# Performance work log

Measured on AMD Instinct MI355X. Metric: run time of the kernel, lower is better.

Reference implementation:

```python
import jax, jax.numpy as jnp
import numpy as np

N_VOCAB = 100000
N_FIELDS = 40
K = 64
ATTN = 64
BATCH = 2048

def setup_inputs() -> dict:
    key = jax.random.key(0)
    ks = jax.random.split(key, 9)
    x = jax.random.randint(ks[0], (BATCH, N_FIELDS), 0, N_VOCAB)
    lin_table = jax.random.normal(ks[1], (N_VOCAB, 1), dtype=jnp.float32) * 0.01
    V_table = jax.random.normal(ks[2], (N_VOCAB, K), dtype=jnp.float32) * 0.01
    W1 = jax.random.normal(ks[3], (K, ATTN), dtype=jnp.float32) * (1.0 / np.sqrt(K))
    b1 = jnp.zeros((ATTN,), dtype=jnp.float32)
    W2 = jax.random.normal(ks[4], (ATTN, 1), dtype=jnp.float32) * (1.0 / np.sqrt(ATTN))
    b2 = jnp.zeros((1,), dtype=jnp.float32)
    Wf = jax.random.normal(ks[5], (K, 1), dtype=jnp.float32) * (1.0 / np.sqrt(K))
    bf = jnp.zeros((1,), dtype=jnp.float32)
    return {"x": x, "lin_table": lin_table, "V_table": V_table,
            "W1": W1, "b1": b1, "W2": W2, "b2": b2, "Wf": Wf, "bf": bf}

def reference(x, lin_table, V_table, W1, b1, W2, b2, Wf, bf):
    # linear part: sum of per-feature scalar weights -> [B, 1]
    linear_part = jnp.sum(lin_table[x], axis=1)
    # embeddings: [B, F, K]
    embd = V_table[x]
    # pairwise interactions: [B, F, F, K]
    pw = embd[:, :, None, :] * embd[:, None, :, :]
    # attention MLP: k -> attn -> 1, scores [B, F, F, 1]
    h = jax.nn.relu(jnp.einsum('bijk,ka->bija', pw, W1) + b1)
    scores = jnp.einsum('bija,ao->bijo', h, W2) + b2
    # softmax over dim=2 (second field axis)
    probs = jax.nn.softmax(scores, axis=2)
    # weighted sum over j then i -> [B, K]
    weighted = jnp.sum(probs * pw, axis=2)
    weighted_embd = jnp.sum(weighted, axis=1)
    interaction_part = weighted_embd @ Wf + bf  # [B, 1]
    return jax.nn.sigmoid(linear_part + interaction_part)[:, 0]
```

## Files before the change

### kernel.cpp

```cpp
#include <hip/hip_runtime.h>

#define NF 40
#define KD 64

typedef float f32x4 __attribute__((ext_vector_type(4)));
typedef _Float16 f16x8 __attribute__((ext_vector_type(8)));
typedef _Float16 f16x4 __attribute__((ext_vector_type(4)));

__global__ __launch_bounds__(256, 4)
void afm_kernel(const int* __restrict__ x,
                const float* __restrict__ lin_table,
                const float* __restrict__ V_table,
                const float* __restrict__ W1,
                const float* __restrict__ b1,
                const float* __restrict__ W2,
                const float* __restrict__ b2,
                const float* __restrict__ Wf,
                const float* __restrict__ bf,
                float* __restrict__ out)
{
    __shared__ _Float16 ew[4][NF][72];
    __shared__ _Float16 Qw[4][48][72];
    __shared__ unsigned short lut[832];

    const int tid = threadIdx.x;
    const int w = tid >> 6;
    const int lane = tid & 63;
    const int l15 = lane & 15;
    const int lhi = lane >> 4;
    const int smp = blockIdx.x * 4 + w;

    for (int p0 = tid; p0 < 832; p0 += 256) {
        int p = p0 > 819 ? 819 : p0;
        int i = (int)((81.0f - sqrtf(6561.0f - 8.0f * (float)p)) * 0.5f);
        int off = (i * (81 - i)) >> 1;
        if ((((i + 1) * (80 - i)) >> 1) <= p) { ++i; off = (i * (81 - i)) >> 1; }
        else if (off > p)                     { --i; off = (i * (81 - i)) >> 1; }
        lut[p0] = (unsigned short)((i << 8) | (i + (p - off)));
    }

    _Float16* e = &ew[w][0][0];
    _Float16* Q = &Qw[w][0][0];

    {
        f16x8 zh = {0, 0, 0, 0, 0, 0, 0, 0};
        for (int t = lane; t < 192; t += 64) {
            if (t < 120) {
                int r = t / 3, c8 = t - r * 3;
                *reinterpret_cast<f16x8*>(Q + r * 72 + 40 + c8 * 8) = zh;
            } else {
                int t2 = t - 120, r9 = t2 / 9;
                *reinterpret_cast<f16x8*>(Q + (40 + r9) * 72 + (t2 - r9 * 9) * 8) = zh;
            }
        }
    }

    for (int q = lane; q < NF * (KD / 4); q += 64) {
        int i = q >> 4, k4 = q & 15;
        int ix = x[smp * NF + i];
        float4 v = reinterpret_cast<const float4*>(V_table + (size_t)ix * KD)[k4];
        f16x4 hv = {(_Float16)v.x, (_Float16)v.y, (_Float16)v.z, (_Float16)v.w};
        *reinterpret_cast<f16x4*>(e + i * 72 + k4 * 4) = hv;
    }
    float linv = (lane < NF) ? lin_table[x[smp * NF + lane]] : 0.0f;

    f16x8 Af[4][2];
    #pragma unroll
    for (int at = 0; at < 4; ++at) {
        #pragma unroll
        for (int ks = 0; ks < 2; ++ks) {
            f16x8 t;
            #pragma unroll
            for (int el = 0; el < 8; ++el)
                t[el] = (_Float16)W1[(ks * 32 + lhi * 8 + el) * KD + at * 16 + l15];
            Af[at][ks] = t;
        }
    }
    f32x4 b1v[4], w2v[4];
    #pragma unroll
    for (int at = 0; at < 4; ++at) {
        b1v[at] = *reinterpret_cast<const f32x4*>(b1 + at * 16 + lhi * 4);
        w2v[at] = *reinterpret_cast<const f32x4*>(W2 + at * 16 + lhi * 4);
    }
    float wfv[4];
    #pragma unroll
    for (int nt = 0; nt < 4; ++nt) wfv[nt] = Wf[nt * 16 + l15];
    const float bf0 = bf[0];

    __syncthreads();
    __builtin_amdgcn_wave_barrier();

    const int k0 = lhi * 8;
    for (int mt = 0; mt < 52; ++mt) {
        const int v = lut[mt * 16 + l15];
        const int i = v >> 8;
        const int j = v & 255;
        const _Float16* ei = e + i * 72;
        const _Float16* ej = e + j * 72;
        f16x8 B0 = (*reinterpret_cast<const f16x8*>(ei + k0)) *
                   (*reinterpret_cast<const f16x8*>(ej + k0));
        f16x8 B1 = (*reinterpret_cast<const f16x8*>(ei + k0 + 32)) *
                   (*reinterpret_cast<const f16x8*>(ej + k0 + 32));

        f32x4 d[4];
        #pragma unroll
        for (int at = 0; at < 4; ++at) {
            d[at] = b1v[at];
            d[at] = __builtin_amdgcn_mfma_f32_16x16x32_f16(Af[at][0], B0, d[at], 0, 0, 0);
            d[at] = __builtin_amdgcn_mfma_f32_16x16x32_f16(Af[at][1], B1, d[at], 0, 0, 0);
        }

        float s = 0.0f;
        #pragma unroll
        for (int at = 0; at < 4; ++at) {
            #pragma unroll
            for (int r = 0; r < 4; ++r)
                s = fmaf(fmaxf(d[at][r], 0.0f), w2v[at][r], s);
        }
        s += __shfl_xor(s, 16, 64);
        s += __shfl_xor(s, 32, 64);
        float qv = __expf(s);
        if (lhi == 0) {
            _Float16 qh = (_Float16)qv;
            Q[i * 72 + j] = qh;
            Q[j * 72 + i] = qh;
        }
    }
    __builtin_amdgcn_wave_barrier();

    float acc4[4] = {0.f, 0.f, 0.f, 0.f};
    #pragma unroll
    for (int mt = 0; mt < 3; ++mt) {
        const _Float16* qrow = Q + (mt * 16 + l15) * 72;
        f16x8 aq0 = *reinterpret_cast<const f16x8*>(qrow + lhi * 8);
        f16x8 aq1 = *reinterpret_cast<const f16x8*>(qrow + 32 + lhi * 8);

        f16x8 one0, one1;
        #pragma unroll
        for (int el = 0; el < 8; ++el) {
            one0[el] = (_Float16)1.0f;
            one1[el] = (lhi == 0) ? (_Float16)1.0f : (_Float16)0.0f;
        }
        f32x4 dz = {0.f, 0.f, 0.f, 0.f};
        dz = __builtin_amdgcn_mfma_f32_16x16x32_f16(aq0, one0, dz, 0, 0, 0);
        dz = __builtin_amdgcn_mfma_f32_16x16x32_f16(aq1, one1, dz, 0, 0, 0);
        float rz[4];
        #pragma unroll
        for (int r = 0; r < 4; ++r) {
            int ii = mt * 16 + lhi * 4 + r;
            rz[r] = (ii < NF) ? __builtin_amdgcn_rcpf(dz[r]) : 0.0f;
        }

        #pragma unroll
        for (int nt = 0; nt < 4; ++nt) {
            const int c = nt * 16 + l15;
            f16x8 bv0, bv1;
            #pragma unroll
            for (int el = 0; el < 8; ++el) {
                bv0[el] = e[(lhi * 8 + el) * 72 + c];
                bv1[el] = (lhi == 0) ? e[(32 + el) * 72 + c]
                                     : (_Float16)0.0f;
            }
            f32x4 dq = {0.f, 0.f, 0.f, 0.f};
            dq = __builtin_amdgcn_mfma_f32_16x16x32_f16(aq0, bv0, dq, 0, 0, 0);
            dq = __builtin_amdgcn_mfma_f32_16x16x32_f16(aq1, bv1, dq, 0, 0, 0);

            float a = 0.0f;
            #pragma unroll
            for (int r = 0; r < 4; ++r) {
                int ii = mt * 16 + lhi * 4 + r;
                int iic = ii > 39 ? 39 : ii;
                a = fmaf((float)e[iic * 72 + c] * dq[r], rz[r], a);
            }
            acc4[nt] += a;
        }
    }

    #pragma unroll
    for (int nt = 0; nt < 4; ++nt) {
        acc4[nt] += __shfl_xor(acc4[nt], 16, 64);
        acc4[nt] += __shfl_xor(acc4[nt], 32, 64);
    }
    float inter = 0.0f;
    #pragma unroll
    for (int nt = 0; nt < 4; ++nt) inter = fmaf(acc4[nt], wfv[nt], inter);
    inter += __shfl_xor(inter, 1, 64);
    inter += __shfl_xor(inter, 2, 64);
    inter += __shfl_xor(inter, 4, 64);
    inter += __shfl_xor(inter, 8, 64);

    linv += __shfl_xor(linv, 32, 64);
    linv += __shfl_xor(linv, 16, 64);
    linv += __shfl_xor(linv, 8, 64);
    linv += __shfl_xor(linv, 4, 64);
    linv += __shfl_xor(linv, 2, 64);
    linv += __shfl_xor(linv, 1, 64);

    if (lane == 0) {
        float z = linv + inter + bf0;
        out[smp] = 1.0f / (1.0f + __expf(-z));
    }
}

extern "C" void kernel_launch(void* const* d_in, const int* in_sizes, int n_in,
                              void* d_out, int out_size, void* d_ws, size_t ws_size,
                              hipStream_t stream) {
    const int*   x         = (const int*)d_in[0];
    const float* lin_table = (const float*)d_in[1];
    const float* V_table   = (const float*)d_in[2];
    const float* W1        = (const float*)d_in[3];
    const float* b1        = (const float*)d_in[4];
    const float* W2        = (const float*)d_in[5];
    const float* b2        = (const float*)d_in[6];
    const float* Wf        = (const float*)d_in[7];
    const float* bf        = (const float*)d_in[8];
    float* out = (float*)d_out;

    const int batch = in_sizes[0] / NF;
    afm_kernel<<<batch / 4, 256, 0, stream>>>(x, lin_table, V_table, W1, b1, W2,
                                              b2, Wf, bf, out);
}
```

Measured before the change: 40.28 us.

## Split each sample across four waves and add transposed embedding copy

```diff
diff --git a/kernel.cpp b/kernel.cpp
--- a/kernel.cpp
+++ b/kernel.cpp
@@ -19,17 +19,26 @@
                 const float* __restrict__ bf,
                 float* __restrict__ out)
 {
-    __shared__ _Float16 ew[4][NF][72];
-    __shared__ _Float16 Qw[4][48][72];
+    __shared__ _Float16 e16[NF][72];
+    __shared__ _Float16 eT16[KD][72];
+    __shared__ _Float16 Q16[48][72];
     __shared__ unsigned short lut[832];
+    __shared__ float wsum[4];
 
+    const int b = blockIdx.x;
     const int tid = threadIdx.x;
     const int w = tid >> 6;
     const int lane = tid & 63;
     const int l15 = lane & 15;
     const int lhi = lane >> 4;
-    const int smp = blockIdx.x * 4 + w;
 
+    {
+        f16x8 zh = {0, 0, 0, 0, 0, 0, 0, 0};
+        for (int t = tid; t < 48 * 72 / 8; t += 256)
+            reinterpret_cast<f16x8*>(&Q16[0][0])[t] = zh;
+        int r = tid >> 2, c8 = tid & 3;
+        *reinterpret_cast<f16x8*>(&eT16[r][40 + 8 * c8]) = zh;
+    }
     for (int p0 = tid; p0 < 832; p0 += 256) {
         int p = p0 > 819 ? 819 : p0;
         int i = (int)((81.0f - sqrtf(6561.0f - 8.0f * (float)p)) * 0.5f);
@@ -39,30 +48,18 @@
         lut[p0] = (unsigned short)((i << 8) | (i + (p - off)));
     }
 
-    _Float16* e = &ew[w][0][0];
-    _Float16* Q = &Qw[w][0][0];
-
-    {
-        f16x8 zh = {0, 0, 0, 0, 0, 0, 0, 0};
-        for (int t = lane; t < 192; t += 64) {
-            if (t < 120) {
-                int r = t / 3, c8 = t - r * 3;
-                *reinterpret_cast<f16x8*>(Q + r * 72 + 40 + c8 * 8) = zh;
-            } else {
-                int t2 = t - 120, r9 = t2 / 9;
-                *reinterpret_cast<f16x8*>(Q + (40 + r9) * 72 + (t2 - r9 * 9) * 8) = zh;
-            }
-        }
-    }
-
-    for (int q = lane; q < NF * (KD / 4); q += 64) {
+    for (int q = tid; q < NF * (KD / 4); q += 256) {
         int i = q >> 4, k4 = q & 15;
-        int ix = x[smp * NF + i];
+        int ix = x[b * NF + i];
         float4 v = reinterpret_cast<const float4*>(V_table + (size_t)ix * KD)[k4];
         f16x4 hv = {(_Float16)v.x, (_Float16)v.y, (_Float16)v.z, (_Float16)v.w};
-        *reinterpret_cast<f16x4*>(e + i * 72 + k4 * 4) = hv;
+        *reinterpret_cast<f16x4*>(&e16[i][k4 * 4]) = hv;
+        eT16[k4 * 4 + 0][i] = hv[0];
+        eT16[k4 * 4 + 1][i] = hv[1];
+        eT16[k4 * 4 + 2][i] = hv[2];
+        eT16[k4 * 4 + 3][i] = hv[3];
     }
-    float linv = (lane < NF) ? lin_table[x[smp * NF + lane]] : 0.0f;
+    float linv = (w == 0 && lane < NF) ? lin_table[x[b * NF + lane]] : 0.0f;
 
     f16x8 Af[4][2];
     #pragma unroll
@@ -82,21 +79,17 @@
         b1v[at] = *reinterpret_cast<const f32x4*>(b1 + at * 16 + lhi * 4);
         w2v[at] = *reinterpret_cast<const f32x4*>(W2 + at * 16 + lhi * 4);
     }
-    float wfv[4];
-    #pragma unroll
-    for (int nt = 0; nt < 4; ++nt) wfv[nt] = Wf[nt * 16 + l15];
+    const float wfv = Wf[w * 16 + l15];
     const float bf0 = bf[0];
-
     __syncthreads();
-    __builtin_amdgcn_wave_barrier();
 
     const int k0 = lhi * 8;
-    for (int mt = 0; mt < 52; ++mt) {
+    for (int mt = w; mt < 52; mt += 4) {
         const int v = lut[mt * 16 + l15];
         const int i = v >> 8;
         const int j = v & 255;
-        const _Float16* ei = e + i * 72;
-        const _Float16* ej = e + j * 72;
+        const _Float16* ei = &e16[i][0];
+        const _Float16* ej = &e16[j][0];
         f16x8 B0 = (*reinterpret_cast<const f16x8*>(ei + k0)) *
                    (*reinterpret_cast<const f16x8*>(ej + k0));
         f16x8 B1 = (*reinterpret_cast<const f16x8*>(ei + k0 + 32)) *
@@ -109,7 +102,6 @@
             d[at] = __builtin_amdgcn_mfma_f32_16x16x32_f16(Af[at][0], B0, d[at], 0, 0, 0);
             d[at] = __builtin_amdgcn_mfma_f32_16x16x32_f16(Af[at][1], B1, d[at], 0, 0, 0);
         }
-
         float s = 0.0f;
         #pragma unroll
         for (int at = 0; at < 4; ++at) {
@@ -122,83 +114,67 @@
         float qv = __expf(s);
         if (lhi == 0) {
             _Float16 qh = (_Float16)qv;
-            Q[i * 72 + j] = qh;
-            Q[j * 72 + i] = qh;
+            Q16[i][j] = qh;
+            Q16[j][i] = qh;
         }
     }
-    __builtin_amdgcn_wave_barrier();
+    __syncthreads();
 
-    float acc4[4] = {0.f, 0.f, 0.f, 0.f};
+    const int c = w * 16 + l15;
+    const f16x8 bv0 = *reinterpret_cast<const f16x8*>(&eT16[c][lhi * 8]);
+    const f16x8 bv1 = *reinterpret_cast<const f16x8*>(&eT16[c][32 + lhi * 8]);
+    f16x8 one0, one1;
+    #pragma unroll
+    for (int el = 0; el < 8; ++el) {
+        one0[el] = (_Float16)1.0f;
+        one1[el] = (lhi == 0) ? (_Float16)1.0f : (_Float16)0.0f;
+    }
+
+    float acc = 0.0f;
     #pragma unroll
     for (int mt = 0; mt < 3; ++mt) {
-        const _Float16* qrow = Q + (mt * 16 + l15) * 72;
+        const _Float16* qrow = &Q16[mt * 16 + l15][0];
         f16x8 aq0 = *reinterpret_cast<const f16x8*>(qrow + lhi * 8);
         f16x8 aq1 = *reinterpret_cast<const f16x8*>(qrow + 32 + lhi * 8);
 
-        f16x8 one0, one1;
-        #pragma unroll
-        for (int el = 0; el < 8; ++el) {
-            one0[el] = (_Float16)1.0f;
-            one1[el] = (lhi == 0) ? (_Float16)1.0f : (_Float16)0.0f;
-        }
         f32x4 dz = {0.f, 0.f, 0.f, 0.f};
         dz = __builtin_amdgcn_mfma_f32_16x16x32_f16(aq0, one0, dz, 0, 0, 0);
         dz = __builtin_amdgcn_mfma_f32_16x16x32_f16(aq1, one1, dz, 0, 0, 0);
-        float rz[4];
+
+        f32x4 dq = {0.f, 0.f, 0.f, 0.f};
+        dq = __builtin_amdgcn_mfma_f32_16x16x32_f16(aq0, bv0, dq, 0, 0, 0);
+        dq = __builtin_amdgcn_mfma_f32_16x16x32_f16(aq1, bv1, dq, 0, 0, 0);
+
+        f16x4 ev4 = *reinterpret_cast<const f16x4*>(&eT16[c][mt * 16 + lhi * 4]);
         #pragma unroll
         for (int r = 0; r < 4; ++r) {
             int ii = mt * 16 + lhi * 4 + r;
-            rz[r] = (ii < NF) ? __builtin_amdgcn_rcpf(dz[r]) : 0.0f;
-        }
-
-        #pragma unroll
-        for (int nt = 0; nt < 4; ++nt) {
-            const int c = nt * 16 + l15;
-            f16x8 bv0, bv1;
-            #pragma unroll
-            for (int el = 0; el < 8; ++el) {
-                bv0[el] = e[(lhi * 8 + el) * 72 + c];
-                bv1[el] = (lhi == 0) ? e[(32 + el) * 72 + c]
-                                     : (_Float16)0.0f;
-            }
-            f32x4 dq = {0.f, 0.f, 0.f, 0.f};
-            dq = __builtin_amdgcn_mfma_f32_16x16x32_f16(aq0, bv0, dq, 0, 0, 0);
-            dq = __builtin_amdgcn_mfma_f32_16x16x32_f16(aq1, bv1, dq, 0, 0, 0);
-
-            float a = 0.0f;
-            #pragma unroll
-            for (int r = 0; r < 4; ++r) {
-                int ii = mt * 16 + lhi * 4 + r;
-                int iic = ii > 39 ? 39 : ii;
-                a = fmaf((float)e[iic * 72 + c] * dq[r], rz[r], a);
-            }
-            acc4[nt] += a;
+            float rz = (ii < NF) ? __builtin_amdgcn_rcpf(dz[r]) : 0.0f;
+            acc = fmaf((float)ev4[r] * dq[r], rz, acc);
         }
     }
 
-    #pragma unroll
-    for (int nt = 0; nt < 4; ++nt) {
-        acc4[nt] += __shfl_xor(acc4[nt], 16, 64);
-        acc4[nt] += __shfl_xor(acc4[nt], 32, 64);
-    }
-    float inter = 0.0f;
-    #pragma unroll
-    for (int nt = 0; nt < 4; ++nt) inter = fmaf(acc4[nt], wfv[nt], inter);
-    inter += __shfl_xor(inter, 1, 64);
-    inter += __shfl_xor(inter, 2, 64);
-    inter += __shfl_xor(inter, 4, 64);
-    inter += __shfl_xor(inter, 8, 64);
+    acc += __shfl_xor(acc, 16, 64);
+    acc += __shfl_xor(acc, 32, 64);
+    float ip = acc * wfv;
+    ip += __shfl_xor(ip, 1, 64);
+    ip += __shfl_xor(ip, 2, 64);
+    ip += __shfl_xor(ip, 4, 64);
+    ip += __shfl_xor(ip, 8, 64);
+    if (lane == 0) wsum[w] = ip;
+    __syncthreads();
 
-    linv += __shfl_xor(linv, 32, 64);
-    linv += __shfl_xor(linv, 16, 64);
-    linv += __shfl_xor(linv, 8, 64);
-    linv += __shfl_xor(linv, 4, 64);
-    linv += __shfl_xor(linv, 2, 64);
-    linv += __shfl_xor(linv, 1, 64);
-
-    if (lane == 0) {
-        float z = linv + inter + bf0;
-        out[smp] = 1.0f / (1.0f + __expf(-z));
+    if (w == 0) {
+        linv += __shfl_xor(linv, 32, 64);
+        linv += __shfl_xor(linv, 16, 64);
+        linv += __shfl_xor(linv, 8, 64);
+        linv += __shfl_xor(linv, 4, 64);
+        linv += __shfl_xor(linv, 2, 64);
+        linv += __shfl_xor(linv, 1, 64);
+        if (lane == 0) {
+            float z = linv + wsum[0] + wsum[1] + wsum[2] + wsum[3] + bf0;
+            out[b] = 1.0f / (1.0f + __expf(-z));
+        }
     }
 }
 
@@ -217,6 +193,6 @@
     float* out = (float*)d_out;
 
     const int batch = in_sizes[0] / NF;
-    afm_kernel<<<batch / 4, 256, 0, stream>>>(x, lin_table, V_table, W1, b1, W2,
-                                              b2, Wf, bf, out);
+    afm_kernel<<<batch, 256, 0, stream>>>(x, lin_table, V_table, W1, b1, W2, b2,
+                                          Wf, bf, out);
 }
```

After: 32.61 us (median of 2 runs). 19.0% less time.
